# Performance work log

Hardware: AMD Instinct MI355X
Metric: run time of the kernel (lower is better)

The kernel has to match this reference:

```python
import jax, jax.numpy as jnp
import numpy as np
import math
from jax import lax

B, C, L = 8, 512, 1024
NCONV, K, H = 4, 7, 8
DH = C // H
EPS = 1e-5
NEG = -1e30


def layer_norm(x, g, b):
    mu = jnp.mean(x, axis=-1, keepdims=True)
    var = jnp.mean(jnp.square(x - mu), axis=-1, keepdims=True)
    return (x - mu) * lax.rsqrt(var + EPS) * g + b


def positional_encoding(d, n):
    pos = jnp.arange(n, dtype=jnp.float32)[:, None]                     # [n,1]
    div = jnp.exp(jnp.arange(0, d, 2, dtype=jnp.float32) * (-math.log(10000.0) / d))
    ang = pos * div                                                      # [n,d/2]
    pe = jnp.zeros((d, n), dtype=jnp.float32)
    pe = pe.at[0::2].set(jnp.sin(ang).T).at[1::2].set(jnp.cos(ang).T)
    return pe                                                            # [d,n]


def setup_inputs() -> dict:
    key = jax.random.key(0)
    ks = jax.random.split(key, 20)
    s = 0.02
    inp = {
        "x": jax.random.normal(ks[0], (B, C, L), jnp.float32),
        "mask": jnp.ones((B, L), jnp.float32),
        # conv stack params (stacked over NCONV layers)
        "dw_w": jax.random.normal(ks[1], (NCONV, C, 1, K), jnp.float32) * s,
        "dw_b": jnp.zeros((NCONV, C), jnp.float32),
        "pw_w": jax.random.normal(ks[2], (NCONV, C, C), jnp.float32) * s,
        "pw_b": jnp.zeros((NCONV, C), jnp.float32),
        "ln_conv_g": jnp.ones((NCONV, C), jnp.float32),
        "ln_conv_b": jnp.zeros((NCONV, C), jnp.float32),
        # attention params (torch Linear layout: [out,in])
        "Wq": jax.random.normal(ks[3], (C, C), jnp.float32) * s,
        "bq": jnp.zeros((C,), jnp.float32),
        "Wk": jax.random.normal(ks[4], (C, C), jnp.float32) * s,
        "bk": jnp.zeros((C,), jnp.float32),
        "Wv": jax.random.normal(ks[5], (C, C), jnp.float32) * s,
        "bv": jnp.zeros((C,), jnp.float32),
        "Wo": jax.random.normal(ks[6], (C, C), jnp.float32) * s,
        "bo": jnp.zeros((C,), jnp.float32),
        "ln_att_g": jnp.ones((C,), jnp.float32),
        "ln_att_b": jnp.zeros((C,), jnp.float32),
        # final fc + its layernorm
        "Wf": jax.random.normal(ks[7], (C, C), jnp.float32) * s,
        "bf": jnp.zeros((C,), jnp.float32),
        "ln_fc_g": jnp.ones((C,), jnp.float32),
        "ln_fc_b": jnp.zeros((C,), jnp.float32),
    }
    return inp


def reference(x, mask, dw_w, dw_b, pw_w, pw_b, ln_conv_g, ln_conv_b,
              Wq, bq, Wk, bk, Wv, bv, Wo, bo, ln_att_g, ln_att_b,
              Wf, bf, ln_fc_g, ln_fc_b):
    # positional encoding on channels-first input, then -> [B,L,C]
    out = x + positional_encoding(C, L)[None]          # [B,C,L]; dropout = eval mode (identity)
    out = out.transpose(0, 2, 1)                       # [B,L,C]
    res = out
    for i in range(NCONV):                             # fixed small layer loop
        h = layer_norm(out, ln_conv_g[i], ln_conv_b[i])
        h = h.transpose(0, 2, 1)                       # [B,C,L]
        h = lax.conv_general_dilated(h, dw_w[i], (1,), [(K // 2, K // 2)],
                                     dimension_numbers=("NCH", "OIH", "NCH"),
                                     feature_group_count=C) + dw_b[i][None, :, None]
        h = jnp.einsum("bcl,oc->bol", h, pw_w[i]) + pw_b[i][None, :, None]
        h = jax.nn.relu(h).transpose(0, 2, 1)          # [B,L,C]
        out = h + res
        res = out
    # masked multi-head self-attention
    a = layer_norm(out, ln_att_g, ln_att_b)
    q = (a @ Wq.T + bq).reshape(B, L, H, DH)
    k = (a @ Wk.T + bk).reshape(B, L, H, DH)
    v = (a @ Wv.T + bv).reshape(B, L, H, DH)
    scale = 1.0 / math.sqrt(DH)
    scores = jnp.einsum("blhd,bmhd->bhlm", q, k) * scale   # [B,H,L,L]
    m = mask[:, None, None, :]                              # mask over keys
    scores = scores * m + (1.0 - m) * NEG
    attn = jax.nn.softmax(scores, axis=-1)
    o = jnp.einsum("bhlm,bmhd->blhd", attn, v).reshape(B, L, C)
    o = o @ Wo.T + bo
    out = o + res
    res = out
    # feed-forward (single Linear + relu) with residual
    f = layer_norm(out, ln_fc_g, ln_fc_b)
    f = jax.nn.relu(f @ Wf.T + bf)
    out = f + res
    return out
```

## Files before the change

### kernel.cpp

```cpp
#include <hip/hip_runtime.h>
#include <hip/hip_bf16.h>

#define L_SEQ 1024
#define CCH   512
#define NB    8

typedef __bf16 bf16_t;
typedef __bf16 bf16x4 __attribute__((ext_vector_type(4)));
typedef __bf16 bf16x8 __attribute__((ext_vector_type(8)));
typedef float  f32x4  __attribute__((ext_vector_type(4)));

__device__ __forceinline__ void gload_lds16(const void* g, void* l) {
  __builtin_amdgcn_global_load_lds((const __attribute__((address_space(1))) void*)g,
                                   (__attribute__((address_space(3))) void*)l, 16, 0, 0);
}

__global__ __launch_bounds__(256) void cvt_kernel(const float* __restrict__ in,
                                                  bf16_t* __restrict__ out, int n) {
  int i = blockIdx.x * 256 + threadIdx.x;
  if (i < n) out[i] = (bf16_t)in[i];
}

__global__ __launch_bounds__(256) void dwt_kernel(const float* __restrict__ in,
                                                  float* __restrict__ out) {
  int idx = blockIdx.x * 256 + threadIdx.x;
  if (idx >= 4 * 7 * 512) return;
  int i = idx / 3584, r = idx % 3584, t = r >> 9, c = r & 511;
  out[idx] = in[i * 3584 + c * 7 + t];
}

__global__ __launch_bounds__(256) void pe_kernel(const float* __restrict__ x,
                                                 float* __restrict__ out) {
  __shared__ float tile[32][33];
  int l0 = blockIdx.x * 32, c0 = blockIdx.y * 32, b = blockIdx.z;
  int tx = threadIdx.x, ty = threadIdx.y;
#pragma unroll
  for (int r = 0; r < 32; r += 8)
    tile[ty + r][tx] = x[(size_t)(b * CCH + c0 + ty + r) * L_SEQ + l0 + tx];
  __syncthreads();
#pragma unroll
  for (int r = 0; r < 32; r += 8) {
    int l = l0 + ty + r, c = c0 + tx;
    float div = expf(-(float)(2 * (c >> 1)) * (9.210340371976184f / 512.0f));
    float ang = (float)l * div;
    float pe = (c & 1) ? cosf(ang) : sinf(ang);
    out[(size_t)(b * L_SEQ + l) * CCH + c] = tile[tx][ty + r] + pe;
  }
}

template <int BF16OUT>
__global__ __launch_bounds__(256) void ln_kernel(const float* __restrict__ in,
                                                 const float* __restrict__ gam,
                                                 const float* __restrict__ bet,
                                                 void* __restrict__ outp) {
  int w = threadIdx.x >> 6, l = threadIdx.x & 63;
  int row = blockIdx.x * 4 + w;
  const float* p = in + (size_t)row * CCH + l * 8;
  float v[8];
  *(float4*)(&v[0]) = *(const float4*)p;
  *(float4*)(&v[4]) = *(const float4*)(p + 4);
  float s = 0.f, s2 = 0.f;
#pragma unroll
  for (int j = 0; j < 8; j++) { s += v[j]; s2 += v[j] * v[j]; }
#pragma unroll
  for (int off = 1; off < 64; off <<= 1) {
    s += __shfl_xor(s, off);
    s2 += __shfl_xor(s2, off);
  }
  float mean = s * (1.0f / 512.0f);
  float var = s2 * (1.0f / 512.0f) - mean * mean;
  float inv = rsqrtf(var + 1e-5f);
  float gv[8], bv[8];
  *(float4*)(&gv[0]) = *(const float4*)(gam + l * 8);
  *(float4*)(&gv[4]) = *(const float4*)(gam + l * 8 + 4);
  *(float4*)(&bv[0]) = *(const float4*)(bet + l * 8);
  *(float4*)(&bv[4]) = *(const float4*)(bet + l * 8 + 4);
  if (BF16OUT) {
    bf16x8 o;
#pragma unroll
    for (int j = 0; j < 8; j++) o[j] = (bf16_t)((v[j] - mean) * inv * gv[j] + bv[j]);
    *(bf16x8*)((bf16_t*)outp + (size_t)row * CCH + l * 8) = o;
  } else {
    float o[8];
#pragma unroll
    for (int j = 0; j < 8; j++) o[j] = (v[j] - mean) * inv * gv[j] + bv[j];
    float* q = (float*)outp + (size_t)row * CCH + l * 8;
    *(float4*)q = *(float4*)&o[0];
    *(float4*)(q + 4) = *(float4*)&o[4];
  }
}

__global__ __launch_bounds__(256) void dw_kernel(const bf16_t* __restrict__ h,
                                                 const float* __restrict__ wtt,
                                                 const float* __restrict__ bias,
                                                 bf16_t* __restrict__ out) {
  int idx = blockIdx.x * 256 + threadIdx.x;
  int cg = idx & 63;
  int row = idx >> 6;
  int l = row & (L_SEQ - 1);
  float acc[8];
  *(float4*)&acc[0] = *(const float4*)(bias + cg * 8);
  *(float4*)&acc[4] = *(const float4*)(bias + cg * 8 + 4);
#pragma unroll
  for (int t = 0; t < 7; t++) {
    int ll = l + t - 3;
    if (ll >= 0 && ll < L_SEQ) {
      bf16x8 hv = *(const bf16x8*)&h[(size_t)(row + t - 3) * CCH + cg * 8];
      float wv[8];
      *(float4*)&wv[0] = *(const float4*)(wtt + t * CCH + cg * 8);
      *(float4*)&wv[4] = *(const float4*)(wtt + t * CCH + cg * 8 + 4);
#pragma unroll
      for (int j = 0; j < 8; j++) acc[j] += (float)hv[j] * wv[j];
    }
  }
  bf16x8 o;
#pragma unroll
  for (int j = 0; j < 8; j++) o[j] = (bf16_t)acc[j];
  *(bf16x8*)&out[(size_t)row * CCH + cg * 8] = o;
}

__device__ __forceinline__ int swz32(int row, int cb) {
  return cb ^ (((row >> 1) & 3) << 4);
}

template <int RELU, int RES, int BF16OUT>
__global__ __launch_bounds__(256) void gemm_kernel(const bf16_t* __restrict__ A,
                                                   const bf16_t* __restrict__ W,
                                                   const float* __restrict__ bias,
                                                   const float* __restrict__ res,
                                                   float* __restrict__ outf,
                                                   bf16_t* __restrict__ outb) {
  __shared__ __align__(16) bf16_t As[64 * 32];
  __shared__ __align__(16) bf16_t Bs[128 * 32];
  int tid = threadIdx.x;
  int w = tid >> 6, l = tid & 63;
  int m0 = blockIdx.x * 64, n0 = blockIdx.y * 128;
  int wr = w >> 1, wc = w & 1;
  int lc = l & 15, lg = l >> 4;
  f32x4 acc[2][4];
#pragma unroll
  for (int i = 0; i < 2; i++)
#pragma unroll
    for (int j = 0; j < 4; j++) acc[i][j] = f32x4{0.f, 0.f, 0.f, 0.f};

  int lrow = l >> 2;
  int lkb = (l & 3) * 16;
  for (int kk = 0; kk < 16; kk++) {
    int k0 = kk * 32;
    {
      int r = w * 16 + lrow;
      int sk = swz32(r, lkb) >> 1;
      gload_lds16(A + (size_t)(m0 + r) * CCH + k0 + sk, &As[w * 512]);
    }
#pragma unroll
    for (int cc = 0; cc < 2; cc++) {
      int r = w * 32 + cc * 16 + lrow;
      int sk = swz32(r, lkb) >> 1;
      gload_lds16(W + (size_t)(n0 + r) * CCH + k0 + sk, &Bs[w * 1024 + cc * 512]);
    }
    __syncthreads();
    bf16x8 fa[2], fb[4];
#pragma unroll
    for (int i = 0; i < 2; i++) {
      int ra = wr * 32 + i * 16 + lc;
      fa[i] = *(const bf16x8*)&As[ra * 32 + (swz32(ra, lg * 16) >> 1)];
    }
#pragma unroll
    for (int j = 0; j < 4; j++) {
      int rb = wc * 64 + j * 16 + lc;
      fb[j] = *(const bf16x8*)&Bs[rb * 32 + (swz32(rb, lg * 16) >> 1)];
    }
#pragma unroll
    for (int i = 0; i < 2; i++)
#pragma unroll
      for (int j = 0; j < 4; j++)
        acc[i][j] = __builtin_amdgcn_mfma_f32_16x16x32_bf16(fa[i], fb[j], acc[i][j], 0, 0, 0);
    __syncthreads();
  }
#pragma unroll
  for (int i = 0; i < 2; i++) {
    int mbase = m0 + wr * 32 + i * 16 + lg * 4;
#pragma unroll
    for (int j = 0; j < 4; j++) {
      int n = n0 + wc * 64 + j * 16 + lc;
      float bn = bias[n];
#pragma unroll
      for (int r = 0; r < 4; r++) {
        int m = mbase + r;
        float v2 = acc[i][j][r] + bn;
        if (RELU) v2 = fmaxf(v2, 0.f);
        if (RES) v2 += res[(size_t)m * CCH + n];
        if (BF16OUT) outb[(size_t)m * CCH + n] = (bf16_t)v2;
        else outf[(size_t)m * CCH + n] = v2;
      }
    }
  }
}

__global__ __launch_bounds__(256) void qkv_kernel(const bf16_t* __restrict__ A,
                                                  const bf16_t* __restrict__ Wqkv,
                                                  const float* __restrict__ bq,
                                                  const float* __restrict__ bk,
                                                  const float* __restrict__ bv,
                                                  bf16_t* __restrict__ QB,
                                                  bf16_t* __restrict__ KB,
                                                  bf16_t* __restrict__ VT) {
  __shared__ __align__(16) bf16_t As[64 * 32];
  __shared__ __align__(16) bf16_t Bs[128 * 32];
  int tid = threadIdx.x;
  int w = tid >> 6, l = tid & 63;
  int m0 = blockIdx.x * 64, n0 = blockIdx.y * 128;
  int sec = n0 >> 9;
  int wr = w >> 1, wc = w & 1;
  int lc = l & 15, lg = l >> 4;
  f32x4 acc[2][4];
#pragma unroll
  for (int i = 0; i < 2; i++)
#pragma unroll
    for (int j = 0; j < 4; j++) acc[i][j] = f32x4{0.f, 0.f, 0.f, 0.f};

  int lrow = l >> 2;
  int lkb = (l & 3) * 16;
  for (int kk = 0; kk < 16; kk++) {
    int k0 = kk * 32;
    {
      int r = w * 16 + lrow;
      int sk = swz32(r, lkb) >> 1;
      gload_lds16(A + (size_t)(m0 + r) * CCH + k0 + sk, &As[w * 512]);
    }
#pragma unroll
    for (int cc = 0; cc < 2; cc++) {
      int r = w * 32 + cc * 16 + lrow;
      int sk = swz32(r, lkb) >> 1;
      gload_lds16(Wqkv + (size_t)(n0 + r) * CCH + k0 + sk, &Bs[w * 1024 + cc * 512]);
    }
    __syncthreads();
    bf16x8 fa[2], fb[4];
#pragma unroll
    for (int i = 0; i < 2; i++) {
      int ra = wr * 32 + i * 16 + lc;
      fa[i] = *(const bf16x8*)&As[ra * 32 + (swz32(ra, lg * 16) >> 1)];
    }
#pragma unroll
    for (int j = 0; j < 4; j++) {
      int rb = wc * 64 + j * 16 + lc;
      fb[j] = *(const bf16x8*)&Bs[rb * 32 + (swz32(rb, lg * 16) >> 1)];
    }
#pragma unroll
    for (int i = 0; i < 2; i++)
#pragma unroll
      for (int j = 0; j < 4; j++)
        acc[i][j] = __builtin_amdgcn_mfma_f32_16x16x32_bf16(fa[i], fb[j], acc[i][j], 0, 0, 0);
    __syncthreads();
  }
  const float* bp = (sec == 0) ? bq : (sec == 1) ? bk : bv;
#pragma unroll
  for (int i = 0; i < 2; i++) {
    int mbase = m0 + wr * 32 + i * 16 + lg * 4;
#pragma unroll
    for (int j = 0; j < 4; j++) {
      int n = n0 + wc * 64 + j * 16 + lc;
      int nl = n & 511;
      float bn = bp[nl];
      if (sec < 2) {
        bf16_t* ob = (sec == 0) ? QB : KB;
#pragma unroll
        for (int r = 0; r < 4; r++)
          ob[(size_t)(mbase + r) * CCH + nl] = (bf16_t)(acc[i][j][r] + bn);
      } else {
        int h = nl >> 6, d = nl & 63;
        int b = mbase >> 10, lpos = mbase & 1023;
        bf16x4 t;
#pragma unroll
        for (int r = 0; r < 4; r++) t[r] = (bf16_t)(acc[i][j][r] + bn);
        *(bf16x4*)&VT[(((size_t)(b * 8 + h) * 64 + d) * L_SEQ) + lpos] = t;
      }
    }
  }
}

__global__ __launch_bounds__(256) void attn_kernel(const bf16_t* __restrict__ Q,
                                                   const bf16_t* __restrict__ K,
                                                   const bf16_t* __restrict__ VT,
                                                   const float* __restrict__ mask,
                                                   bf16_t* __restrict__ O) {
  __shared__ __align__(16) bf16_t Ks[64 * 64];
  __shared__ __align__(16) bf16_t Vs[64 * 64];
  __shared__ __align__(16) bf16_t Pl[4][16 * 64];
  int tid = threadIdx.x;
  int w = tid >> 6, l = tid & 63;
  int bid = blockIdx.x;
  int sw = (bid & 7) * 128 + (bid >> 3);
  int qb = sw & 15, h = (sw >> 4) & 7, b = sw >> 7;
  int lg = l >> 4, lc = l & 15;

  int qrow = qb * 64 + w * 16 + lc;
  const bf16_t* qptr = Q + ((size_t)(b * L_SEQ + qrow) * CCH + h * 64);
  bf16x8 qf0 = *(const bf16x8*)(qptr + lg * 8);
  bf16x8 qf1 = *(const bf16x8*)(qptr + 32 + lg * 8);

  f32x4 oacc[4];
  float psl[4] = {0.f, 0.f, 0.f, 0.f};
#pragma unroll
  for (int nf = 0; nf < 4; nf++) oacc[nf] = f32x4{0.f, 0.f, 0.f, 0.f};

  int srow = l >> 3;
  int scb = (l & 7) * 16;

  for (int kc = 0; kc < 16; kc++) {
#pragma unroll
    for (int r = 0; r < 2; r++) {
      int row = r * 32 + w * 8 + srow;
      int sc = (scb ^ ((row & 7) << 4)) >> 1;
      int key = kc * 64 + row;
      gload_lds16(K + ((size_t)(b * L_SEQ + key) * CCH + h * 64 + sc),
                  &Ks[(r * 32 + w * 8) * 64]);
      gload_lds16(VT + (((size_t)(b * 8 + h) * 64 + row) * L_SEQ + kc * 64 + sc),
                  &Vs[(r * 32 + w * 8) * 64]);
    }
    __syncthreads();

    f32x4 sacc[4];
#pragma unroll
    for (int kf = 0; kf < 4; kf++) sacc[kf] = f32x4{0.f, 0.f, 0.f, 0.f};
#pragma unroll
    for (int kf = 0; kf < 4; kf++) {
      int row = kf * 16 + lc;
      int s = (row & 7) << 4;
      const bf16_t* kr = &Ks[row * 64];
      bf16x8 b0 = *(const bf16x8*)(kr + (((lg * 16) ^ s) >> 1));
      sacc[kf] = __builtin_amdgcn_mfma_f32_16x16x32_bf16(qf0, b0, sacc[kf], 0, 0, 0);
      bf16x8 b1 = *(const bf16x8*)(kr + (((64 + lg * 16) ^ s) >> 1));
      sacc[kf] = __builtin_amdgcn_mfma_f32_16x16x32_bf16(qf1, b1, sacc[kf], 0, 0, 0);
    }

#pragma unroll
    for (int kf = 0; kf < 4; kf++) {
      float mv = mask[b * L_SEQ + kc * 64 + kf * 16 + lc];
      float mneg = (1.f - mv) * (-1e30f);
      float msc = 0.125f * mv;
#pragma unroll
      for (int j = 0; j < 4; j++) {
        float p = __expf(sacc[kf][j] * msc + mneg);
        psl[j] += p;
        int q = lg * 4 + j;
        int cb = (kf * 32 + lc * 2) ^ ((q & 7) << 4);
        Pl[w][(q * 128 + cb) >> 1] = (bf16_t)p;
      }
    }

    int sp = (lc & 7) << 4;
    bf16x8 pa0 = *(const bf16x8*)&Pl[w][(lc * 128 + ((lg * 16) ^ sp)) >> 1];
    bf16x8 pa1 = *(const bf16x8*)&Pl[w][(lc * 128 + ((64 + lg * 16) ^ sp)) >> 1];
#pragma unroll
    for (int nf = 0; nf < 4; nf++) {
      int d = nf * 16 + lc;
      int s = (d & 7) << 4;
      const bf16_t* vr = &Vs[d * 64];
      bf16x8 vb0 = *(const bf16x8*)(vr + (((lg * 16) ^ s) >> 1));
      oacc[nf] = __builtin_amdgcn_mfma_f32_16x16x32_bf16(pa0, vb0, oacc[nf], 0, 0, 0);
      bf16x8 vb1 = *(const bf16x8*)(vr + (((64 + lg * 16) ^ s) >> 1));
      oacc[nf] = __builtin_amdgcn_mfma_f32_16x16x32_bf16(pa1, vb1, oacc[nf], 0, 0, 0);
    }
    __syncthreads();
  }

#pragma unroll
  for (int off = 1; off < 16; off <<= 1)
#pragma unroll
    for (int j = 0; j < 4; j++) psl[j] += __shfl_xor(psl[j], off);

#pragma unroll
  for (int j = 0; j < 4; j++) {
    float is = 1.0f / psl[j];
    int r = qb * 64 + w * 16 + lg * 4 + j;
    bf16_t* op = O + ((size_t)(b * L_SEQ + r) * CCH + h * 64);
#pragma unroll
    for (int nf = 0; nf < 4; nf++) op[nf * 16 + lc] = (bf16_t)(oacc[nf][j] * is);
  }
}

extern "C" void kernel_launch(void* const* d_in, const int* in_sizes, int n_in,
                              void* d_out, int out_size, void* d_ws, size_t ws_size,
                              hipStream_t stream) {
  const float* x = (const float*)d_in[0];
  const float* mask = (const float*)d_in[1];
  const float* dw_w = (const float*)d_in[2];
  const float* dw_b = (const float*)d_in[3];
  const float* pw_w = (const float*)d_in[4];
  const float* pw_b = (const float*)d_in[5];
  const float* ln_conv_g = (const float*)d_in[6];
  const float* ln_conv_b = (const float*)d_in[7];
  const float* Wq = (const float*)d_in[8];  const float* bq = (const float*)d_in[9];
  const float* Wk = (const float*)d_in[10]; const float* bk = (const float*)d_in[11];
  const float* Wv = (const float*)d_in[12]; const float* bv = (const float*)d_in[13];
  const float* Wo = (const float*)d_in[14]; const float* bo = (const float*)d_in[15];
  const float* ln_att_g = (const float*)d_in[16]; const float* ln_att_b = (const float*)d_in[17];
  const float* Wf = (const float*)d_in[18]; const float* bfc = (const float*)d_in[19];
  const float* ln_fc_g = (const float*)d_in[20]; const float* ln_fc_b = (const float*)d_in[21];

  float* OUT = (float*)d_out;

  char* ws = (char*)d_ws;
  bf16_t* HBUF = (bf16_t*)(ws);
  bf16_t* ABF  = (bf16_t*)(ws + (8u << 20));
  bf16_t* QB   = (bf16_t*)(ws + (16u << 20));
  bf16_t* KB   = (bf16_t*)(ws + (24u << 20));
  bf16_t* VT   = (bf16_t*)(ws + (32u << 20));
  bf16_t* WPW  = (bf16_t*)(ws + (40u << 20));
  bf16_t* WQKV = WPW + 4 * 262144;
  bf16_t* WOB  = WQKV + 3 * 262144;
  bf16_t* WFB  = WOB + 262144;
  float*  WT   = (float*)(WFB + 262144);

  cvt_kernel<<<4096, 256, 0, stream>>>(pw_w, WPW, 4 * 262144);
  cvt_kernel<<<1024, 256, 0, stream>>>(Wq, WQKV, 262144);
  cvt_kernel<<<1024, 256, 0, stream>>>(Wk, WQKV + 262144, 262144);
  cvt_kernel<<<1024, 256, 0, stream>>>(Wv, WQKV + 2 * 262144, 262144);
  cvt_kernel<<<1024, 256, 0, stream>>>(Wo, WOB, 262144);
  cvt_kernel<<<1024, 256, 0, stream>>>(Wf, WFB, 262144);
  dwt_kernel<<<56, 256, 0, stream>>>(dw_w, WT);

  pe_kernel<<<dim3(32, 16, NB), dim3(32, 8), 0, stream>>>(x, OUT);

  dim3 ggrid(128, 4);
  for (int i = 0; i < 4; i++) {
    ln_kernel<1><<<2048, 256, 0, stream>>>(OUT, ln_conv_g + i * 512, ln_conv_b + i * 512, HBUF);
    dw_kernel<<<2048, 256, 0, stream>>>(HBUF, WT + i * 3584, dw_b + i * 512, ABF);
    gemm_kernel<1, 1, 0><<<ggrid, 256, 0, stream>>>(ABF, WPW + i * 262144, pw_b + i * 512,
                                                    OUT, OUT, nullptr);
  }
  ln_kernel<1><<<2048, 256, 0, stream>>>(OUT, ln_att_g, ln_att_b, ABF);
  qkv_kernel<<<dim3(128, 12), 256, 0, stream>>>(ABF, WQKV, bq, bk, bv, QB, KB, VT);
  attn_kernel<<<1024, 256, 0, stream>>>(QB, KB, VT, mask, ABF);
  gemm_kernel<0, 1, 0><<<ggrid, 256, 0, stream>>>(ABF, WOB, bo, OUT, OUT, nullptr);
  ln_kernel<1><<<2048, 256, 0, stream>>>(OUT, ln_fc_g, ln_fc_b, ABF);
  gemm_kernel<1, 1, 0><<<ggrid, 256, 0, stream>>>(ABF, WFB, bfc, OUT, (float*)d_out, nullptr);
}
```

Baseline: 343.3 us.

## Fuse LayerNorm stats into GEMM epilogues, double-buffer GEMMs, merge conversion kernels

The separate LayerNorm kernels are replaced by row-statistics partial sums written from the GEMM epilogues (and a stats kernel after the positional encoding). The depthwise conv now applies LayerNorm on the fly from fp32 input, so the intermediate bf16 buffer goes away. The GEMM and QKV kernels move to a K=64 tile with double-buffered LDS, overlapping loads with MFMA work. Weight conversion is merged into one launch, and the positional table is precomputed once. The trade-off is more LDS per block, one-pass variance with its numeric risk, and the conv re-reading seven fp32 rows.

```diff
diff --git a/kernel.cpp b/kernel.cpp
--- a/kernel.cpp
+++ b/kernel.cpp
@@ -15,21 +15,43 @@
                                    (__attribute__((address_space(3))) void*)l, 16, 0, 0);
 }
 
-__global__ __launch_bounds__(256) void cvt_kernel(const float* __restrict__ in,
-                                                  bf16_t* __restrict__ out, int n) {
-  int i = blockIdx.x * 256 + threadIdx.x;
-  if (i < n) out[i] = (bf16_t)in[i];
-}
-
-__global__ __launch_bounds__(256) void dwt_kernel(const float* __restrict__ in,
-                                                  float* __restrict__ out) {
+__global__ __launch_bounds__(256) void cvtall_kernel(
+    const float* __restrict__ pw_w, const float* __restrict__ Wq,
+    const float* __restrict__ Wk, const float* __restrict__ Wv,
+    const float* __restrict__ Wo, const float* __restrict__ Wf,
+    const float* __restrict__ dw_w,
+    bf16_t* __restrict__ WPW, bf16_t* __restrict__ WQKV,
+    bf16_t* __restrict__ WOB, bf16_t* __restrict__ WFB,
+    float* __restrict__ WT) {
   int idx = blockIdx.x * 256 + threadIdx.x;
-  if (idx >= 4 * 7 * 512) return;
-  int i = idx / 3584, r = idx % 3584, t = r >> 9, c = r & 511;
-  out[idx] = in[i * 3584 + c * 7 + t];
+  if (idx < 1048576) { WPW[idx] = (bf16_t)pw_w[idx]; return; }
+  idx -= 1048576;
+  if (idx < 262144) { WQKV[idx] = (bf16_t)Wq[idx]; return; }
+  idx -= 262144;
+  if (idx < 262144) { WQKV[262144 + idx] = (bf16_t)Wk[idx]; return; }
+  idx -= 262144;
+  if (idx < 262144) { WQKV[524288 + idx] = (bf16_t)Wv[idx]; return; }
+  idx -= 262144;
+  if (idx < 262144) { WOB[idx] = (bf16_t)Wo[idx]; return; }
+  idx -= 262144;
+  if (idx < 262144) { WFB[idx] = (bf16_t)Wf[idx]; return; }
+  idx -= 262144;
+  if (idx < 14336) {
+    int i = idx / 3584, r = idx % 3584, t = r >> 9, c = r & 511;
+    WT[idx] = dw_w[i * 3584 + c * 7 + t];
+  }
+}
+
+__global__ __launch_bounds__(256) void pet_kernel(float* __restrict__ PET) {
+  int idx = blockIdx.x * 256 + threadIdx.x;
+  int l = idx >> 9, c = idx & 511;
+  float div = expf(-(float)(2 * (c >> 1)) * (9.210340371976184f / 512.0f));
+  float ang = (float)l * div;
+  PET[idx] = (c & 1) ? cosf(ang) : sinf(ang);
 }
 
 __global__ __launch_bounds__(256) void pe_kernel(const float* __restrict__ x,
+                                                 const float* __restrict__ PET,
                                                  float* __restrict__ out) {
   __shared__ float tile[32][33];
   int l0 = blockIdx.x * 32, c0 = blockIdx.y * 32, b = blockIdx.z;
@@ -41,141 +63,191 @@
 #pragma unroll
   for (int r = 0; r < 32; r += 8) {
     int l = l0 + ty + r, c = c0 + tx;
-    float div = expf(-(float)(2 * (c >> 1)) * (9.210340371976184f / 512.0f));
-    float ang = (float)l * div;
-    float pe = (c & 1) ? cosf(ang) : sinf(ang);
-    out[(size_t)(b * L_SEQ + l) * CCH + c] = tile[tx][ty + r] + pe;
-  }
-}
-
-template <int BF16OUT>
-__global__ __launch_bounds__(256) void ln_kernel(const float* __restrict__ in,
-                                                 const float* __restrict__ gam,
-                                                 const float* __restrict__ bet,
-                                                 void* __restrict__ outp) {
+    out[(size_t)(b * L_SEQ + l) * CCH + c] = tile[tx][ty + r] + PET[l * CCH + c];
+  }
+}
+
+__global__ __launch_bounds__(256) void stats_kernel(const float* __restrict__ in,
+                                                    float* __restrict__ Psum,
+                                                    float* __restrict__ Psq) {
   int w = threadIdx.x >> 6, l = threadIdx.x & 63;
   int row = blockIdx.x * 4 + w;
   const float* p = in + (size_t)row * CCH + l * 8;
   float v[8];
   *(float4*)(&v[0]) = *(const float4*)p;
   *(float4*)(&v[4]) = *(const float4*)(p + 4);
-  float s = 0.f, s2 = 0.f;
-#pragma unroll
-  for (int j = 0; j < 8; j++) { s += v[j]; s2 += v[j] * v[j]; }
-#pragma unroll
-  for (int off = 1; off < 64; off <<= 1) {
-    s += __shfl_xor(s, off);
-    s2 += __shfl_xor(s2, off);
-  }
-  float mean = s * (1.0f / 512.0f);
-  float var = s2 * (1.0f / 512.0f) - mean * mean;
+  float s = 0.f, q = 0.f;
+#pragma unroll
+  for (int j = 0; j < 8; j++) { s += v[j]; q += v[j] * v[j]; }
+  s += __shfl_xor(s, 1); q += __shfl_xor(q, 1);
+  s += __shfl_xor(s, 2); q += __shfl_xor(q, 2);
+  s += __shfl_xor(s, 4); q += __shfl_xor(q, 4);
+  if ((l & 7) == 0) {
+    Psum[row * 8 + (l >> 3)] = s;
+    Psq[row * 8 + (l >> 3)] = q;
+  }
+}
+
+__global__ __launch_bounds__(256) void ln_apply_kernel(const float* __restrict__ in,
+                                                       const float* __restrict__ Psum,
+                                                       const float* __restrict__ Psq,
+                                                       const float* __restrict__ gam,
+                                                       const float* __restrict__ bet,
+                                                       bf16_t* __restrict__ out) {
+  int w = threadIdx.x >> 6, l = threadIdx.x & 63;
+  int row = blockIdx.x * 4 + w;
+  float v0 = 0.f;
+  if (l < 8) v0 = Psum[row * 8 + l];
+  else if (l < 16) v0 = Psq[row * 8 + (l - 8)];
+  v0 += __shfl_xor(v0, 1); v0 += __shfl_xor(v0, 2); v0 += __shfl_xor(v0, 4);
+  float sum = __shfl(v0, 0), sq = __shfl(v0, 8);
+  float mean = sum * (1.0f / 512.0f);
+  float var = sq * (1.0f / 512.0f) - mean * mean;
   float inv = rsqrtf(var + 1e-5f);
-  float gv[8], bv[8];
+  const float* p = in + (size_t)row * CCH + l * 8;
+  float v[8], gv[8], bv[8];
+  *(float4*)(&v[0]) = *(const float4*)p;
+  *(float4*)(&v[4]) = *(const float4*)(p + 4);
   *(float4*)(&gv[0]) = *(const float4*)(gam + l * 8);
   *(float4*)(&gv[4]) = *(const float4*)(gam + l * 8 + 4);
   *(float4*)(&bv[0]) = *(const float4*)(bet + l * 8);
   *(float4*)(&bv[4]) = *(const float4*)(bet + l * 8 + 4);
-  if (BF16OUT) {
-    bf16x8 o;
-#pragma unroll
-    for (int j = 0; j < 8; j++) o[j] = (bf16_t)((v[j] - mean) * inv * gv[j] + bv[j]);
-    *(bf16x8*)((bf16_t*)outp + (size_t)row * CCH + l * 8) = o;
-  } else {
-    float o[8];
-#pragma unroll
-    for (int j = 0; j < 8; j++) o[j] = (v[j] - mean) * inv * gv[j] + bv[j];
-    float* q = (float*)outp + (size_t)row * CCH + l * 8;
-    *(float4*)q = *(float4*)&o[0];
-    *(float4*)(q + 4) = *(float4*)&o[4];
-  }
-}
-
-__global__ __launch_bounds__(256) void dw_kernel(const bf16_t* __restrict__ h,
-                                                 const float* __restrict__ wtt,
-                                                 const float* __restrict__ bias,
-                                                 bf16_t* __restrict__ out) {
+  bf16x8 o;
+#pragma unroll
+  for (int j = 0; j < 8; j++) o[j] = (bf16_t)((v[j] - mean) * inv * gv[j] + bv[j]);
+  *(bf16x8*)(out + (size_t)row * CCH + l * 8) = o;
+}
+
+__global__ __launch_bounds__(256) void dwln_kernel(const float* __restrict__ in,
+                                                   const float* __restrict__ Psum,
+                                                   const float* __restrict__ Psq,
+                                                   const float* __restrict__ gam,
+                                                   const float* __restrict__ bet,
+                                                   const float* __restrict__ wtt,
+                                                   const float* __restrict__ dbias,
+                                                   bf16_t* __restrict__ out) {
   int idx = blockIdx.x * 256 + threadIdx.x;
-  int cg = idx & 63;
+  int lane = threadIdx.x & 63;
   int row = idx >> 6;
   int l = row & (L_SEQ - 1);
-  float acc[8];
-  *(float4*)&acc[0] = *(const float4*)(bias + cg * 8);
-  *(float4*)&acc[4] = *(const float4*)(bias + cg * 8 + 4);
+  float m_ = 0.f, i_ = 0.f;
+  if (lane < 7) {
+    int ll = l + lane - 3;
+    if (ll >= 0 && ll < L_SEQ) {
+      int rr = row + lane - 3;
+      float s = 0.f, q = 0.f;
+#pragma unroll
+      for (int c = 0; c < 8; c++) { s += Psum[rr * 8 + c]; q += Psq[rr * 8 + c]; }
+      float mm = s * (1.0f / 512.0f);
+      m_ = mm;
+      i_ = rsqrtf(q * (1.0f / 512.0f) - mm * mm + 1e-5f);
+    }
+  }
+  float gv[8], bv[8], acc[8];
+  *(float4*)&gv[0] = *(const float4*)(gam + lane * 8);
+  *(float4*)&gv[4] = *(const float4*)(gam + lane * 8 + 4);
+  *(float4*)&bv[0] = *(const float4*)(bet + lane * 8);
+  *(float4*)&bv[4] = *(const float4*)(bet + lane * 8 + 4);
+  *(float4*)&acc[0] = *(const float4*)(dbias + lane * 8);
+  *(float4*)&acc[4] = *(const float4*)(dbias + lane * 8 + 4);
 #pragma unroll
   for (int t = 0; t < 7; t++) {
+    float mt = __shfl(m_, t), it = __shfl(i_, t);
     int ll = l + t - 3;
     if (ll >= 0 && ll < L_SEQ) {
-      bf16x8 hv = *(const bf16x8*)&h[(size_t)(row + t - 3) * CCH + cg * 8];
-      float wv[8];
-      *(float4*)&wv[0] = *(const float4*)(wtt + t * CCH + cg * 8);
-      *(float4*)&wv[4] = *(const float4*)(wtt + t * CCH + cg * 8 + 4);
-#pragma unroll
-      for (int j = 0; j < 8; j++) acc[j] += (float)hv[j] * wv[j];
+      const float* p = in + (size_t)(row + t - 3) * CCH + lane * 8;
+      float v[8], wv[8];
+      *(float4*)&v[0] = *(const float4*)p;
+      *(float4*)&v[4] = *(const float4*)(p + 4);
+      *(float4*)&wv[0] = *(const float4*)(wtt + t * CCH + lane * 8);
+      *(float4*)&wv[4] = *(const float4*)(wtt + t * CCH + lane * 8 + 4);
+#pragma unroll
+      for (int j = 0; j < 8; j++)
+        acc[j] += ((v[j] - mt) * it * gv[j] + bv[j]) * wv[j];
     }
   }
   bf16x8 o;
 #pragma unroll
   for (int j = 0; j < 8; j++) o[j] = (bf16_t)acc[j];
-  *(bf16x8*)&out[(size_t)row * CCH + cg * 8] = o;
-}
-
-__device__ __forceinline__ int swz32(int row, int cb) {
-  return cb ^ (((row >> 1) & 3) << 4);
-}
-
-template <int RELU, int RES, int BF16OUT>
+  *(bf16x8*)&out[(size_t)row * CCH + lane * 8] = o;
+}
+
+#define GEMM_STAGE(SRCA, SRCB, BI, K0)                                            \
+  do {                                                                            \
+    _Pragma("unroll") for (int cc = 0; cc < 2; cc++) {                            \
+      int row_ = cc * 32 + w * 8 + srow;                                          \
+      int off_ = (scb ^ ((row_ & 7) << 4)) >> 1;                                  \
+      gload_lds16(SRCA + (size_t)(m0 + row_) * CCH + (K0) + off_,                 \
+                  &As[BI][(cc * 32 + w * 8) * 64]);                               \
+    }                                                                             \
+    _Pragma("unroll") for (int cc = 0; cc < 4; cc++) {                            \
+      int row_ = cc * 32 + w * 8 + srow;                                          \
+      int off_ = (scb ^ ((row_ & 7) << 4)) >> 1;                                  \
+      gload_lds16(SRCB + (size_t)(n0 + row_) * CCH + (K0) + off_,                 \
+                  &Bs[BI][(cc * 32 + w * 8) * 64]);                               \
+    }                                                                             \
+  } while (0)
+
+#define GEMM_COMPUTE(BI)                                                          \
+  do {                                                                            \
+    _Pragma("unroll") for (int ks = 0; ks < 2; ks++) {                            \
+      bf16x8 fa[2], fb[4];                                                        \
+      _Pragma("unroll") for (int i = 0; i < 2; i++) {                             \
+        int ra = wr * 32 + i * 16 + lc;                                           \
+        fa[i] = *(const bf16x8*)&As[BI][ra * 64 +                                 \
+                 (((ks * 64 + lg * 16) ^ ((ra & 7) << 4)) >> 1)];                 \
+      }                                                                           \
+      _Pragma("unroll") for (int j = 0; j < 4; j++) {                             \
+        int rb = wc * 64 + j * 16 + lc;                                           \
+        fb[j] = *(const bf16x8*)&Bs[BI][rb * 64 +                                 \
+                 (((ks * 64 + lg * 16) ^ ((rb & 7) << 4)) >> 1)];                 \
+      }                                                                           \
+      _Pragma("unroll") for (int i = 0; i < 2; i++)                               \
+        _Pragma("unroll") for (int j = 0; j < 4; j++)                             \
+          acc[i][j] = __builtin_amdgcn_mfma_f32_16x16x32_bf16(fa[i], fb[j],       \
+                                                              acc[i][j], 0, 0, 0);\
+    }                                                                             \
+  } while (0)
+
+template <int RELU, int RES, int BF16OUT, int STATS>
 __global__ __launch_bounds__(256) void gemm_kernel(const bf16_t* __restrict__ A,
                                                    const bf16_t* __restrict__ W,
                                                    const float* __restrict__ bias,
                                                    const float* __restrict__ res,
                                                    float* __restrict__ outf,
-                                                   bf16_t* __restrict__ outb) {
-  __shared__ __align__(16) bf16_t As[64 * 32];
-  __shared__ __align__(16) bf16_t Bs[128 * 32];
+                                                   bf16_t* __restrict__ outb,
+                                                   float* __restrict__ Psum,
+                                                   float* __restrict__ Psq) {
+  __shared__ __align__(16) bf16_t As[2][64 * 64];
+  __shared__ __align__(16) bf16_t Bs[2][128 * 64];
   int tid = threadIdx.x;
   int w = tid >> 6, l = tid & 63;
   int m0 = blockIdx.x * 64, n0 = blockIdx.y * 128;
   int wr = w >> 1, wc = w & 1;
   int lc = l & 15, lg = l >> 4;
+  int srow = l >> 3, scb = (l & 7) * 16;
   f32x4 acc[2][4];
 #pragma unroll
   for (int i = 0; i < 2; i++)
 #pragma unroll
     for (int j = 0; j < 4; j++) acc[i][j] = f32x4{0.f, 0.f, 0.f, 0.f};
 
-  int lrow = l >> 2;
-  int lkb = (l & 3) * 16;
-  for (int kk = 0; kk < 16; kk++) {
-    int k0 = kk * 32;
-    {
-      int r = w * 16 + lrow;
-      int sk = swz32(r, lkb) >> 1;
-      gload_lds16(A + (size_t)(m0 + r) * CCH + k0 + sk, &As[w * 512]);
-    }
-#pragma unroll
-    for (int cc = 0; cc < 2; cc++) {
-      int r = w * 32 + cc * 16 + lrow;
-      int sk = swz32(r, lkb) >> 1;
-      gload_lds16(W + (size_t)(n0 + r) * CCH + k0 + sk, &Bs[w * 1024 + cc * 512]);
-    }
+  GEMM_STAGE(A, W, 0, 0);
+  __syncthreads();
+  int cur = 0;
+  for (int t = 0; t < 8; t++) {
+    if (t < 7) GEMM_STAGE(A, W, cur ^ 1, (t + 1) * 64);
+    GEMM_COMPUTE(cur);
     __syncthreads();
-    bf16x8 fa[2], fb[4];
-#pragma unroll
-    for (int i = 0; i < 2; i++) {
-      int ra = wr * 32 + i * 16 + lc;
-      fa[i] = *(const bf16x8*)&As[ra * 32 + (swz32(ra, lg * 16) >> 1)];
-    }
-#pragma unroll
-    for (int j = 0; j < 4; j++) {
-      int rb = wc * 64 + j * 16 + lc;
-      fb[j] = *(const bf16x8*)&Bs[rb * 32 + (swz32(rb, lg * 16) >> 1)];
-    }
+    cur ^= 1;
+  }
+
+  float ps[2][4], pq[2][4];
+  if (STATS) {
 #pragma unroll
     for (int i = 0; i < 2; i++)
 #pragma unroll
-      for (int j = 0; j < 4; j++)
-        acc[i][j] = __builtin_amdgcn_mfma_f32_16x16x32_bf16(fa[i], fb[j], acc[i][j], 0, 0, 0);
-    __syncthreads();
+      for (int r = 0; r < 4; r++) { ps[i][r] = 0.f; pq[i][r] = 0.f; }
   }
 #pragma unroll
   for (int i = 0; i < 2; i++) {
@@ -192,8 +264,27 @@
         if (RES) v2 += res[(size_t)m * CCH + n];
         if (BF16OUT) outb[(size_t)m * CCH + n] = (bf16_t)v2;
         else outf[(size_t)m * CCH + n] = v2;
+        if (STATS) { ps[i][r] += v2; pq[i][r] += v2 * v2; }
       }
     }
+  }
+  if (STATS) {
+    int chunk = blockIdx.y * 2 + wc;
+#pragma unroll
+    for (int i = 0; i < 2; i++)
+#pragma unroll
+      for (int r = 0; r < 4; r++) {
+        float s = ps[i][r], q = pq[i][r];
+        s += __shfl_xor(s, 1); q += __shfl_xor(q, 1);
+        s += __shfl_xor(s, 2); q += __shfl_xor(q, 2);
+        s += __shfl_xor(s, 4); q += __shfl_xor(q, 4);
+        s += __shfl_xor(s, 8); q += __shfl_xor(q, 8);
+        if (lc == 0) {
+          int row = m0 + wr * 32 + i * 16 + lg * 4 + r;
+          Psum[row * 8 + chunk] = s;
+          Psq[row * 8 + chunk] = q;
+        }
+      }
   }
 }
 
@@ -205,54 +296,31 @@
                                                   bf16_t* __restrict__ QB,
                                                   bf16_t* __restrict__ KB,
                                                   bf16_t* __restrict__ VT) {
-  __shared__ __align__(16) bf16_t As[64 * 32];
-  __shared__ __align__(16) bf16_t Bs[128 * 32];
+  __shared__ __align__(16) bf16_t As[2][64 * 64];
+  __shared__ __align__(16) bf16_t Bs[2][128 * 64];
   int tid = threadIdx.x;
   int w = tid >> 6, l = tid & 63;
   int m0 = blockIdx.x * 64, n0 = blockIdx.y * 128;
   int sec = n0 >> 9;
   int wr = w >> 1, wc = w & 1;
   int lc = l & 15, lg = l >> 4;
+  int srow = l >> 3, scb = (l & 7) * 16;
   f32x4 acc[2][4];
 #pragma unroll
   for (int i = 0; i < 2; i++)
 #pragma unroll
     for (int j = 0; j < 4; j++) acc[i][j] = f32x4{0.f, 0.f, 0.f, 0.f};
 
-  int lrow = l >> 2;
-  int lkb = (l & 3) * 16;
-  for (int kk = 0; kk < 16; kk++) {
-    int k0 = kk * 32;
-    {
-      int r = w * 16 + lrow;
-      int sk = swz32(r, lkb) >> 1;
-      gload_lds16(A + (size_t)(m0 + r) * CCH + k0 + sk, &As[w * 512]);
-    }
-#pragma unroll
-    for (int cc = 0; cc < 2; cc++) {
-      int r = w * 32 + cc * 16 + lrow;
-      int sk = swz32(r, lkb) >> 1;
-      gload_lds16(Wqkv + (size_t)(n0 + r) * CCH + k0 + sk, &Bs[w * 1024 + cc * 512]);
-    }
+  GEMM_STAGE(A, Wqkv, 0, 0);
+  __syncthreads();
+  int cur = 0;
+  for (int t = 0; t < 8; t++) {
+    if (t < 7) GEMM_STAGE(A, Wqkv, cur ^ 1, (t + 1) * 64);
+    GEMM_COMPUTE(cur);
     __syncthreads();
-    bf16x8 fa[2], fb[4];
-#pragma unroll
-    for (int i = 0; i < 2; i++) {
-      int ra = wr * 32 + i * 16 + lc;
-      fa[i] = *(const bf16x8*)&As[ra * 32 + (swz32(ra, lg * 16) >> 1)];
-    }
-#pragma unroll
-    for (int j = 0; j < 4; j++) {
-      int rb = wc * 64 + j * 16 + lc;
-      fb[j] = *(const bf16x8*)&Bs[rb * 32 + (swz32(rb, lg * 16) >> 1)];
-    }
-#pragma unroll
-    for (int i = 0; i < 2; i++)
-#pragma unroll
-      for (int j = 0; j < 4; j++)
-        acc[i][j] = __builtin_amdgcn_mfma_f32_16x16x32_bf16(fa[i], fb[j], acc[i][j], 0, 0, 0);
-    __syncthreads();
-  }
+    cur ^= 1;
+  }
+
   const float* bp = (sec == 0) ? bq : (sec == 1) ? bk : bv;
 #pragma unroll
   for (int i = 0; i < 2; i++) {
@@ -402,38 +470,42 @@
   float* OUT = (float*)d_out;
 
   char* ws = (char*)d_ws;
-  bf16_t* HBUF = (bf16_t*)(ws);
-  bf16_t* ABF  = (bf16_t*)(ws + (8u << 20));
-  bf16_t* QB   = (bf16_t*)(ws + (16u << 20));
-  bf16_t* KB   = (bf16_t*)(ws + (24u << 20));
-  bf16_t* VT   = (bf16_t*)(ws + (32u << 20));
-  bf16_t* WPW  = (bf16_t*)(ws + (40u << 20));
-  bf16_t* WQKV = WPW + 4 * 262144;
-  bf16_t* WOB  = WQKV + 3 * 262144;
-  bf16_t* WFB  = WOB + 262144;
-  float*  WT   = (float*)(WFB + 262144);
-
-  cvt_kernel<<<4096, 256, 0, stream>>>(pw_w, WPW, 4 * 262144);
-  cvt_kernel<<<1024, 256, 0, stream>>>(Wq, WQKV, 262144);
-  cvt_kernel<<<1024, 256, 0, stream>>>(Wk, WQKV + 262144, 262144);
-  cvt_kernel<<<1024, 256, 0, stream>>>(Wv, WQKV + 2 * 262144, 262144);
-  cvt_kernel<<<1024, 256, 0, stream>>>(Wo, WOB, 262144);
-  cvt_kernel<<<1024, 256, 0, stream>>>(Wf, WFB, 262144);
-  dwt_kernel<<<56, 256, 0, stream>>>(dw_w, WT);
-
-  pe_kernel<<<dim3(32, 16, NB), dim3(32, 8), 0, stream>>>(x, OUT);
+  bf16_t* ABF  = (bf16_t*)(ws);
+  bf16_t* QB   = (bf16_t*)(ws + (8u << 20));
+  bf16_t* KB   = (bf16_t*)(ws + (16u << 20));
+  bf16_t* VT   = (bf16_t*)(ws + (24u << 20));
+  char*   wb   = ws + (32u << 20);
+  bf16_t* WPW  = (bf16_t*)(wb);
+  bf16_t* WQKV = (bf16_t*)(wb + (2u << 20));
+  bf16_t* WOB  = (bf16_t*)(wb + 3584u * 1024);
+  bf16_t* WFB  = (bf16_t*)(wb + (4u << 20));
+  float*  WT   = (float*)(wb + 4608u * 1024);
+  float*  PET  = (float*)(ws + (37u << 20));
+  float*  Psum = (float*)(ws + (39u << 20));
+  float*  Psq  = (float*)(ws + (39u << 20) + 262144);
+
+  cvtall_kernel<<<9272, 256, 0, stream>>>(pw_w, Wq, Wk, Wv, Wo, Wf, dw_w,
+                                          WPW, WQKV, WOB, WFB, WT);
+  pet_kernel<<<2048, 256, 0, stream>>>(PET);
+  pe_kernel<<<dim3(32, 16, NB), dim3(32, 8), 0, stream>>>(x, PET, OUT);
+  stats_kernel<<<2048, 256, 0, stream>>>(OUT, Psum, Psq);
 
   dim3 ggrid(128, 4);
   for (int i = 0; i < 4; i++) {
-    ln_kernel<1><<<2048, 256, 0, stream>>>(OUT, ln_conv_g + i * 512, ln_conv_b + i * 512, HBUF);
-    dw_kernel<<<2048, 256, 0, stream>>>(HBUF, WT + i * 3584, dw_b + i * 512, ABF);
-    gemm_kernel<1, 1, 0><<<ggrid, 256, 0, stream>>>(ABF, WPW + i * 262144, pw_b + i * 512,
-                                                    OUT, OUT, nullptr);
-  }
-  ln_kernel<1><<<2048, 256, 0, stream>>>(OUT, ln_att_g, ln_att_b, ABF);
+    dwln_kernel<<<2048, 256, 0, stream>>>(OUT, Psum, Psq, ln_conv_g + i * 512,
+                                          ln_conv_b + i * 512, WT + i * 3584,
+                                          dw_b + i * 512, ABF);
+    gemm_kernel<1, 1, 0, 1><<<ggrid, 256, 0, stream>>>(ABF, WPW + i * 262144,
+                                                       pw_b + i * 512, OUT, OUT,
+                                                       nullptr, Psum, Psq);
+  }
+  ln_apply_kernel<<<2048, 256, 0, stream>>>(OUT, Psum, Psq, ln_att_g, ln_att_b, ABF);
   qkv_kernel<<<dim3(128, 12), 256, 0, stream>>>(ABF, WQKV, bq, bk, bv, QB, KB, VT);
   attn_kernel<<<1024, 256, 0, stream>>>(QB, KB, VT, mask, ABF);
-  gemm_kernel<0, 1, 0><<<ggrid, 256, 0, stream>>>(ABF, WOB, bo, OUT, OUT, nullptr);
-  ln_kernel<1><<<2048, 256, 0, stream>>>(OUT, ln_fc_g, ln_fc_b, ABF);
-  gemm_kernel<1, 1, 0><<<ggrid, 256, 0, stream>>>(ABF, WFB, bfc, OUT, (float*)d_out, nullptr);
-}
+  gemm_kernel<0, 1, 0, 1><<<ggrid, 256, 0, stream>>>(ABF, WOB, bo, OUT, OUT,
+                                                     nullptr, Psum, Psq);
+  ln_apply_kernel<<<2048, 256, 0, stream>>>(OUT, Psum, Psq, ln_fc_g, ln_fc_b, ABF);
+  gemm_kernel<1, 1, 0, 0><<<ggrid, 256, 0, stream>>>(ABF, WFB, bfc, OUT,
+                                                     (float*)d_out, nullptr,
+                                                     nullptr, nullptr);
+}
```

New measurement: 353.1 us. +2.8%, slower.
